# Kernel tuning notes

Hardware: AMD Instinct MI355X
Metric: run time of the kernel (lower is better)

## Reference

```python
import jax, jax.numpy as jnp
import numpy as np

B, LQ, LK, H = 4, 256, 512, 256

def setup_inputs() -> dict:
    key = jax.random.key(0)
    ks = jax.random.split(key, 9)
    return {
        "query": jax.random.normal(ks[0], (B, LQ, H), dtype=jnp.float32),
        "key": jax.random.normal(ks[1], (B, LK, H), dtype=jnp.float32),
        "value": jax.random.normal(ks[2], (B, LK, H), dtype=jnp.float32),
        "mask": jax.random.randint(ks[3], (B, LK), 0, 2, dtype=jnp.int32),
        "Wq": jax.random.normal(ks[4], (H, H), dtype=jnp.float32) / np.sqrt(H),
        "bq": jnp.zeros((H,), dtype=jnp.float32),
        "Wk": jax.random.normal(ks[5], (H, H), dtype=jnp.float32) / np.sqrt(H),
        "bk": jnp.zeros((H,), dtype=jnp.float32),
        "v": jax.random.normal(ks[6], (H,), dtype=jnp.float32) / np.sqrt(H),
        "bv": jnp.zeros((), dtype=jnp.float32),
    }

def reference(query, key, value, mask, Wq, bq, Wk, bk, v, bv):
    # Linear projections: y = x @ W^T + b (torch nn.Linear convention)
    q = query @ Wq.T + bq            # [B, Lq, H]
    k = key @ Wk.T + bk              # [B, Lk, H]
    # Broadcast add -> tanh -> project to scalar with v
    s = jnp.tanh(q[:, :, None, :] + k[:, None, :, :])   # [B, Lq, Lk, H]
    scores = jnp.einsum('bqkh,h->bqk', s, v) + bv        # [B, Lq, Lk]
    scores = jnp.where(mask[:, None, :] == 0, -jnp.inf, scores)
    attn_weights = jax.nn.softmax(scores, axis=-1)       # [B, Lq, Lk]
    attn_output = jnp.einsum('bqk,bkh->bqh', attn_weights, value)
    return (attn_output, attn_weights)
```

## Files before the change

### kernel.cpp

```cpp
#include <hip/hip_runtime.h>
#include <math.h>

#define NB  4
#define NLQ 256
#define NLK 512
#define NH  256

#define SCALE_2LOG2E 2.885390081777927f
#define LOG2E        1.4426950408889634f

__global__ __launch_bounds__(256) void setup_kernel(
    const float* __restrict__ Wq, const float* __restrict__ Wk,
    const int* __restrict__ mask,
    float* __restrict__ Wtq, float* __restrict__ Wtk,
    int* __restrict__ act, int* __restrict__ nact)
{
    const int blk = blockIdx.x;
    const int t   = threadIdx.x;

    if (blk < 32) {
        __shared__ float ts[64][65];
        const int m    = blk >> 4;
        const int tile = blk & 15;
        const int h0 = (tile >> 2) * 64;
        const int c0 = (tile & 3) * 64;
        const float* W  = m ? Wk  : Wq;
        float*       Wt = m ? Wtk : Wtq;
        const int lr = t >> 4, lc = t & 15;
        #pragma unroll
        for (int i = 0; i < 4; ++i) {
            const int r = lr + 16 * i;
            const float4 d = *(const float4*)(W + (size_t)(h0 + r) * NH + c0 + lc * 4);
            ts[r][lc * 4 + 0] = d.x;
            ts[r][lc * 4 + 1] = d.y;
            ts[r][lc * 4 + 2] = d.z;
            ts[r][lc * 4 + 3] = d.w;
        }
        __syncthreads();
        #pragma unroll
        for (int i = 0; i < 4; ++i) {
            const int c = lr + 16 * i;
            float4 d;
            d.x = ts[lc * 4 + 0][c];
            d.y = ts[lc * 4 + 1][c];
            d.z = ts[lc * 4 + 2][c];
            d.w = ts[lc * 4 + 3][c];
            *(float4*)(Wt + (size_t)(c0 + c) * NH + h0 + lc * 4) = d;
        }
    } else if (blk < 32 + NB) {
        const int b = blk - 32;
        __shared__ int wcnt[8], wpre[9];
        const int lane = t & 63, wave = t >> 6;
        const int k1 = t, k2 = t + 256;
        const int m1 = mask[b * NLK + k1];
        const int m2 = mask[b * NLK + k2];
        const unsigned long long below = (1ULL << lane) - 1ULL;
        const unsigned long long bal1 = __ballot(m1 != 0);
        const unsigned long long bal2 = __ballot(m2 != 0);
        const int r1 = __popcll(bal1 & below);
        const int r2 = __popcll(bal2 & below);
        if (lane == 0) { wcnt[wave] = __popcll(bal1); wcnt[4 + wave] = __popcll(bal2); }
        __syncthreads();
        if (t == 0) {
            int s = 0;
            #pragma unroll
            for (int w = 0; w < 8; ++w) { wpre[w] = s; s += wcnt[w]; }
            wpre[8] = s;
        }
        __syncthreads();
        const int na = wpre[8];
        if (m1) act[b * NLK + wpre[wave]     + r1] = k1;
        if (m2) act[b * NLK + wpre[4 + wave] + r2] = k2;
        if (k1 >= na) act[b * NLK + k1] = 0;
        if (k2 >= na) act[b * NLK + k2] = 0;
        if (t == 0) nact[b] = na;
    }
}

__global__ __launch_bounds__(256) void prep_kernel(
    const float* __restrict__ query, const float* __restrict__ key,
    const float* __restrict__ Wtq, const float* __restrict__ bq,
    const float* __restrict__ Wtk, const float* __restrict__ bk,
    const int* __restrict__ act, const int* __restrict__ nact,
    float* __restrict__ qp, float* __restrict__ kp_ct)
{
    const int blk  = blockIdx.x;
    const int t    = threadIdx.x;
    const int wave = t >> 6;
    const int lane = t & 63;

    __shared__ float  xs[4][NH];
    __shared__ float4 ps[4][4][64];
    __shared__ int    ridx[4];

    const float *Wt, *bias;
    int b = 0, j0 = 0, r0 = 0, na = 0;
    const bool isq = (blk < NB * NLQ / 4);

    if (isq) {
        b  = blk & 3;
        r0 = b * NLQ + (blk >> 2) * 4;
        ((float4*)&xs[0][0])[t] = ((const float4*)(query + (size_t)r0 * NH))[t];
        Wt = Wtq; bias = bq;
    } else {
        const int idx = blk - 256;
        b  = idx & 3;
        j0 = (idx >> 2) * 4;
        na = nact[b];
        if (j0 >= na) return;
        if (t < 4) ridx[t] = act[b * NLK + ((j0 + t < na) ? (j0 + t) : j0)];
        __syncthreads();
        const int r = t >> 6, c4 = t & 63;
        ((float4*)xs[r])[c4] =
            ((const float4*)(key + ((size_t)b * NLK + ridx[r]) * NH))[c4];
        Wt = Wtk; bias = bk;
    }
    __syncthreads();

    float4 acc[4];
    #pragma unroll
    for (int r = 0; r < 4; ++r) acc[r] = (float4){0.f, 0.f, 0.f, 0.f};

    const int cbase = wave * 64;
    #pragma unroll 4
    for (int cc = 0; cc < 64; ++cc) {
        const int c = cbase + cc;
        const float4 w = *(const float4*)(Wt + (size_t)c * NH + lane * 4);
        #pragma unroll
        for (int r = 0; r < 4; ++r) {
            const float xv = xs[r][c];
            acc[r].x = fmaf(xv, w.x, acc[r].x);
            acc[r].y = fmaf(xv, w.y, acc[r].y);
            acc[r].z = fmaf(xv, w.z, acc[r].z);
            acc[r].w = fmaf(xv, w.w, acc[r].w);
        }
    }
    #pragma unroll
    for (int r = 0; r < 4; ++r) ps[wave][r][lane] = acc[r];
    __syncthreads();

    const int r = wave, l = lane;
    const float4 p0 = ps[0][r][l], p1 = ps[1][r][l];
    const float4 p2 = ps[2][r][l], p3 = ps[3][r][l];
    const float4 bb = *(const float4*)(bias + l * 4);
    float4 o;
    o.x = (p0.x + p1.x + p2.x + p3.x + bb.x) * SCALE_2LOG2E;
    o.y = (p0.y + p1.y + p2.y + p3.y + bb.y) * SCALE_2LOG2E;
    o.z = (p0.z + p1.z + p2.z + p3.z + bb.z) * SCALE_2LOG2E;
    o.w = (p0.w + p1.w + p2.w + p3.w + bb.w) * SCALE_2LOG2E;
    o.x = __builtin_amdgcn_exp2f(o.x);
    o.y = __builtin_amdgcn_exp2f(o.y);
    o.z = __builtin_amdgcn_exp2f(o.z);
    o.w = __builtin_amdgcn_exp2f(o.w);

    if (isq) {
        *(float4*)(qp + (size_t)(r0 + r) * NH + l * 4) = o;
    } else if (j0 + r < na) {
        const int j = j0 + r;
        kp_ct[((size_t)b * NH + l * 4 + 0) * NLK + j] = o.x;
        kp_ct[((size_t)b * NH + l * 4 + 1) * NLK + j] = o.y;
        kp_ct[((size_t)b * NH + l * 4 + 2) * NLK + j] = o.z;
        kp_ct[((size_t)b * NH + l * 4 + 3) * NLK + j] = o.w;
    }
}

__global__ __launch_bounds__(512) void attn_kernel(
    const float* __restrict__ qp, const float* __restrict__ kp_ct,
    const float* __restrict__ value, const int* __restrict__ mask,
    const int* __restrict__ act, const int* __restrict__ nact,
    const float* __restrict__ vvec,
    float* __restrict__ out_o, float* __restrict__ out_w)
{
    __shared__ float sc0[NLK], sc1[NLK];
    __shared__ int   actl[NLK];
    __shared__ float eqs[2][NH];
    __shared__ float vvs[NH];
    __shared__ float4 buf4[2048];

    const int blk  = blockIdx.x;
    const int b    = blk & 3;
    const int q0   = (blk >> 2) * 2;
    const int t    = threadIdx.x;
    const int lane = t & 63;
    const int wave = t >> 6;

    const int na = nact[b];
    actl[t] = (t < na) ? act[b * NLK + t] : 0;
    if (t < NH) {
        eqs[0][t] = qp[(size_t)(b * NLQ + q0) * NH + t];
        eqs[1][t] = qp[(size_t)(b * NLQ + q0 + 1) * NH + t];
        vvs[t]    = vvec[t];
    }

    float* w0row = out_w + (size_t)(b * NLQ + q0) * NLK;
    float* w1row = w0row + NLK;
    if (!mask[b * NLK + t]) { w0row[t] = 0.f; w1row[t] = 0.f; }
    __syncthreads();

    const int cb = wave * 32;
    const float* kb  = kp_ct + ((size_t)b * NH + cb) * NLK;
    const float* eq0 = &eqs[0][cb];
    const float* eq1 = &eqs[1][cb];
    const float* vv  = &vvs[cb];

    float4 a0 = {0.f, 0.f, 0.f, 0.f}, a1 = {0.f, 0.f, 0.f, 0.f};
    float4 a2 = {0.f, 0.f, 0.f, 0.f}, a3 = {0.f, 0.f, 0.f, 0.f};
    if (na > 256) {
        #pragma unroll 4
        for (int c = 0; c < 32; ++c) {
            const float4 k1 = *(const float4*)(kb + (size_t)c * NLK + 4 * lane);
            const float4 k2 = *(const float4*)(kb + (size_t)c * NLK + 256 + 4 * lane);
            const float eqa = eq0[c];
            const float eqb = eq1[c];
            const float vh  = vv[c];
            a0.x = fmaf(vh, __builtin_amdgcn_rcpf(fmaf(eqa, k1.x, 1.f)), a0.x);
            a0.y = fmaf(vh, __builtin_amdgcn_rcpf(fmaf(eqa, k1.y, 1.f)), a0.y);
            a0.z = fmaf(vh, __builtin_amdgcn_rcpf(fmaf(eqa, k1.z, 1.f)), a0.z);
            a0.w = fmaf(vh, __builtin_amdgcn_rcpf(fmaf(eqa, k1.w, 1.f)), a0.w);
            a1.x = fmaf(vh, __builtin_amdgcn_rcpf(fmaf(eqb, k1.x, 1.f)), a1.x);
            a1.y = fmaf(vh, __builtin_amdgcn_rcpf(fmaf(eqb, k1.y, 1.f)), a1.y);
            a1.z = fmaf(vh, __builtin_amdgcn_rcpf(fmaf(eqb, k1.z, 1.f)), a1.z);
            a1.w = fmaf(vh, __builtin_amdgcn_rcpf(fmaf(eqb, k1.w, 1.f)), a1.w);
            a2.x = fmaf(vh, __builtin_amdgcn_rcpf(fmaf(eqa, k2.x, 1.f)), a2.x);
            a2.y = fmaf(vh, __builtin_amdgcn_rcpf(fmaf(eqa, k2.y, 1.f)), a2.y);
            a2.z = fmaf(vh, __builtin_amdgcn_rcpf(fmaf(eqa, k2.z, 1.f)), a2.z);
            a2.w = fmaf(vh, __builtin_amdgcn_rcpf(fmaf(eqa, k2.w, 1.f)), a2.w);
            a3.x = fmaf(vh, __builtin_amdgcn_rcpf(fmaf(eqb, k2.x, 1.f)), a3.x);
            a3.y = fmaf(vh, __builtin_amdgcn_rcpf(fmaf(eqb, k2.y, 1.f)), a3.y);
            a3.z = fmaf(vh, __builtin_amdgcn_rcpf(fmaf(eqb, k2.z, 1.f)), a3.z);
            a3.w = fmaf(vh, __builtin_amdgcn_rcpf(fmaf(eqb, k2.w, 1.f)), a3.w);
        }
    } else {
        #pragma unroll 4
        for (int c = 0; c < 32; ++c) {
            const float4 k1 = *(const float4*)(kb + (size_t)c * NLK + 4 * lane);
            const float eqa = eq0[c];
            const float eqb = eq1[c];
            const float vh  = vv[c];
            a0.x = fmaf(vh, __builtin_amdgcn_rcpf(fmaf(eqa, k1.x, 1.f)), a0.x);
            a0.y = fmaf(vh, __builtin_amdgcn_rcpf(fmaf(eqa, k1.y, 1.f)), a0.y);
            a0.z = fmaf(vh, __builtin_amdgcn_rcpf(fmaf(eqa, k1.z, 1.f)), a0.z);
            a0.w = fmaf(vh, __builtin_amdgcn_rcpf(fmaf(eqa, k1.w, 1.f)), a0.w);
            a1.x = fmaf(vh, __builtin_amdgcn_rcpf(fmaf(eqb, k1.x, 1.f)), a1.x);
            a1.y = fmaf(vh, __builtin_amdgcn_rcpf(fmaf(eqb, k1.y, 1.f)), a1.y);
            a1.z = fmaf(vh, __builtin_amdgcn_rcpf(fmaf(eqb, k1.z, 1.f)), a1.z);
            a1.w = fmaf(vh, __builtin_amdgcn_rcpf(fmaf(eqb, k1.w, 1.f)), a1.w);
        }
    }
    buf4[(0 * 8 + wave) * 128 + lane]      = a0;
    buf4[(0 * 8 + wave) * 128 + 64 + lane] = a2;
    buf4[(1 * 8 + wave) * 128 + lane]      = a1;
    buf4[(1 * 8 + wave) * 128 + 64 + lane] = a3;
    __syncthreads();
    {
        const float* pf = (const float*)buf4;
        float sA = 0.f, sB = 0.f;
        #pragma unroll
        for (int o = 0; o < 8; ++o) {
            sA += pf[o * 512 + t];
            sB += pf[(8 + o) * 512 + t];
        }
        sc0[t] = (t < na) ? -2.f * sA : -INFINITY;
        sc1[t] = (t < na) ? -2.f * sB : -INFINITY;
    }
    __syncthreads();

    if (wave < 2) {
        float* row = wave ? sc1 : sc0;
        float vals[8];
        float m = -INFINITY;
        #pragma unroll
        for (int j8 = 0; j8 < 8; ++j8) {
            vals[j8] = row[lane + j8 * 64];
            m = fmaxf(m, vals[j8]);
        }
        #pragma unroll
        for (int s = 32; s >= 1; s >>= 1)
            m = fmaxf(m, __shfl_xor(m, s, 64));
        float sum = 0.0f;
        #pragma unroll
        for (int j8 = 0; j8 < 8; ++j8) {
            vals[j8] = __builtin_amdgcn_exp2f((vals[j8] - m) * LOG2E);
            sum += vals[j8];
        }
        #pragma unroll
        for (int s = 32; s >= 1; s >>= 1)
            sum += __shfl_xor(sum, s, 64);
        const float inv = __builtin_amdgcn_rcpf(sum);
        float* wout = out_w + (size_t)(b * NLQ + q0 + wave) * NLK;
        #pragma unroll
        for (int j8 = 0; j8 < 8; ++j8) {
            const int jj = lane + j8 * 64;
            const float w = vals[j8] * inv;
            row[jj] = w;
            if (jj < na) wout[actl[jj]] = w;
        }
    }
    __syncthreads();

    {
        const int c4 = lane * 4;
        const float* vb = value + (size_t)b * NLK * NH + c4;
        float4 o0 = {0.f, 0.f, 0.f, 0.f}, o1 = {0.f, 0.f, 0.f, 0.f};
        #pragma unroll 4
        for (int j = wave; j < na; j += 8) {
            const float w0 = sc0[j];
            const float w1 = sc1[j];
            const int   rj = actl[j];
            const float4 v4 = *(const float4*)(vb + (size_t)rj * NH);
            o0.x = fmaf(w0, v4.x, o0.x); o0.y = fmaf(w0, v4.y, o0.y);
            o0.z = fmaf(w0, v4.z, o0.z); o0.w = fmaf(w0, v4.w, o0.w);
            o1.x = fmaf(w1, v4.x, o1.x); o1.y = fmaf(w1, v4.y, o1.y);
            o1.z = fmaf(w1, v4.z, o1.z); o1.w = fmaf(w1, v4.w, o1.w);
        }
        buf4[t]       = o0;
        buf4[512 + t] = o1;
        __syncthreads();
        if (t < 128) {
            const int row = t >> 6;
            const int l   = t & 63;
            float4 o = buf4[row * 512 + l];
            #pragma unroll
            for (int w = 1; w < 8; ++w) {
                const float4 s = buf4[row * 512 + l + 64 * w];
                o.x += s.x; o.y += s.y; o.z += s.z; o.w += s.w;
            }
            *(float4*)(out_o + (size_t)(b * NLQ + q0 + row) * NH + l * 4) = o;
        }
    }
}

extern "C" void kernel_launch(void* const* d_in, const int* in_sizes, int n_in,
                              void* d_out, int out_size, void* d_ws, size_t ws_size,
                              hipStream_t stream) {
    const float* query = (const float*)d_in[0];
    const float* key   = (const float*)d_in[1];
    const float* value = (const float*)d_in[2];
    const int*   mask  = (const int*)  d_in[3];
    const float* Wq    = (const float*)d_in[4];
    const float* bq    = (const float*)d_in[5];
    const float* Wk    = (const float*)d_in[6];
    const float* bk    = (const float*)d_in[7];
    const float* v     = (const float*)d_in[8];

    float* out_o = (float*)d_out;
    float* out_w = out_o + NB * NLQ * NH;

    float* qp    = (float*)d_ws;
    float* kp_ct = qp + NB * NLQ * NH;
    int*   act   = (int*)(kp_ct + NB * NH * NLK);
    int*   nact  = act + NB * NLK;

    const size_t base = (size_t)(NB * NLQ * NH) + (size_t)(NB * NH * NLK)
                      + NB * NLK + NB;
    float* wtq;
    if (ws_size >= (base + 2 * NH * NH) * sizeof(float)) {
        wtq = (float*)d_ws + base;
    } else {
        wtq = out_w + (size_t)NB * NLQ * NLK - 2 * NH * NH;
    }
    float* wtk = wtq + NH * NH;

    setup_kernel<<<36, 256, 0, stream>>>(Wq, Wk, mask, wtq, wtk, act, nact);
    prep_kernel<<<NB * NLQ / 4 + NB * NLK / 4, 256, 0, stream>>>(
        query, key, wtq, bq, wtk, bk, act, nact, qp, kp_ct);
    attn_kernel<<<NB * NLQ / 2, 512, 0, stream>>>(
        qp, kp_ct, value, mask, act, nact, v, out_o, out_w);
}
```

Before: 106.8 us.

## Process one query row per attention block instead of two

The attention kernel now handles a single query row per block and launches twice as many blocks. Each block does half the tanh/score work and uses half the shared memory and accumulator registers, which should raise occupancy and spread work across more CUs. In exchange, each block still reloads the full projected-key tile and the value rows, so global/L2 traffic for keys and values doubles. An extra barrier is also added before the output reduction buffer is reused.

```diff
diff --git a/kernel.cpp b/kernel.cpp
--- a/kernel.cpp
+++ b/kernel.cpp
@@ -171,15 +171,15 @@
     const float* __restrict__ vvec,
     float* __restrict__ out_o, float* __restrict__ out_w)
 {
-    __shared__ float sc0[NLK], sc1[NLK];
+    __shared__ float sc[NLK];
     __shared__ int   actl[NLK];
-    __shared__ float eqs[2][NH];
+    __shared__ float eqs[NH];
     __shared__ float vvs[NH];
-    __shared__ float4 buf4[2048];
+    __shared__ float4 buf4[1024];
 
     const int blk  = blockIdx.x;
     const int b    = blk & 3;
-    const int q0   = (blk >> 2) * 2;
+    const int q    = blk >> 2;
     const int t    = threadIdx.x;
     const int lane = t & 63;
     const int wave = t >> 6;
@@ -187,91 +187,68 @@
     const int na = nact[b];
     actl[t] = (t < na) ? act[b * NLK + t] : 0;
     if (t < NH) {
-        eqs[0][t] = qp[(size_t)(b * NLQ + q0) * NH + t];
-        eqs[1][t] = qp[(size_t)(b * NLQ + q0 + 1) * NH + t];
-        vvs[t]    = vvec[t];
-    }
-
-    float* w0row = out_w + (size_t)(b * NLQ + q0) * NLK;
-    float* w1row = w0row + NLK;
-    if (!mask[b * NLK + t]) { w0row[t] = 0.f; w1row[t] = 0.f; }
+        eqs[t] = qp[(size_t)(b * NLQ + q) * NH + t];
+        vvs[t] = vvec[t];
+    }
+
+    float* wrow = out_w + (size_t)(b * NLQ + q) * NLK;
+    if (!mask[b * NLK + t]) wrow[t] = 0.f;
     __syncthreads();
 
     const int cb = wave * 32;
-    const float* kb  = kp_ct + ((size_t)b * NH + cb) * NLK;
-    const float* eq0 = &eqs[0][cb];
-    const float* eq1 = &eqs[1][cb];
-    const float* vv  = &vvs[cb];
-
-    float4 a0 = {0.f, 0.f, 0.f, 0.f}, a1 = {0.f, 0.f, 0.f, 0.f};
-    float4 a2 = {0.f, 0.f, 0.f, 0.f}, a3 = {0.f, 0.f, 0.f, 0.f};
+    const float* kb = kp_ct + ((size_t)b * NH + cb) * NLK;
+    const float* eq = &eqs[cb];
+    const float* vv = &vvs[cb];
+
+    float4 a0 = {0.f, 0.f, 0.f, 0.f};
+    float4 a1 = {0.f, 0.f, 0.f, 0.f};
     if (na > 256) {
         #pragma unroll 4
         for (int c = 0; c < 32; ++c) {
             const float4 k1 = *(const float4*)(kb + (size_t)c * NLK + 4 * lane);
             const float4 k2 = *(const float4*)(kb + (size_t)c * NLK + 256 + 4 * lane);
-            const float eqa = eq0[c];
-            const float eqb = eq1[c];
-            const float vh  = vv[c];
-            a0.x = fmaf(vh, __builtin_amdgcn_rcpf(fmaf(eqa, k1.x, 1.f)), a0.x);
-            a0.y = fmaf(vh, __builtin_amdgcn_rcpf(fmaf(eqa, k1.y, 1.f)), a0.y);
-            a0.z = fmaf(vh, __builtin_amdgcn_rcpf(fmaf(eqa, k1.z, 1.f)), a0.z);
-            a0.w = fmaf(vh, __builtin_amdgcn_rcpf(fmaf(eqa, k1.w, 1.f)), a0.w);
-            a1.x = fmaf(vh, __builtin_amdgcn_rcpf(fmaf(eqb, k1.x, 1.f)), a1.x);
-            a1.y = fmaf(vh, __builtin_amdgcn_rcpf(fmaf(eqb, k1.y, 1.f)), a1.y);
-            a1.z = fmaf(vh, __builtin_amdgcn_rcpf(fmaf(eqb, k1.z, 1.f)), a1.z);
-            a1.w = fmaf(vh, __builtin_amdgcn_rcpf(fmaf(eqb, k1.w, 1.f)), a1.w);
-            a2.x = fmaf(vh, __builtin_amdgcn_rcpf(fmaf(eqa, k2.x, 1.f)), a2.x);
-            a2.y = fmaf(vh, __builtin_amdgcn_rcpf(fmaf(eqa, k2.y, 1.f)), a2.y);
-            a2.z = fmaf(vh, __builtin_amdgcn_rcpf(fmaf(eqa, k2.z, 1.f)), a2.z);
-            a2.w = fmaf(vh, __builtin_amdgcn_rcpf(fmaf(eqa, k2.w, 1.f)), a2.w);
-            a3.x = fmaf(vh, __builtin_amdgcn_rcpf(fmaf(eqb, k2.x, 1.f)), a3.x);
-            a3.y = fmaf(vh, __builtin_amdgcn_rcpf(fmaf(eqb, k2.y, 1.f)), a3.y);
-            a3.z = fmaf(vh, __builtin_amdgcn_rcpf(fmaf(eqb, k2.z, 1.f)), a3.z);
-            a3.w = fmaf(vh, __builtin_amdgcn_rcpf(fmaf(eqb, k2.w, 1.f)), a3.w);
+            const float e  = eq[c];
+            const float vh = vv[c];
+            a0.x = fmaf(vh, __builtin_amdgcn_rcpf(fmaf(e, k1.x, 1.f)), a0.x);
+            a0.y = fmaf(vh, __builtin_amdgcn_rcpf(fmaf(e, k1.y, 1.f)), a0.y);
+            a0.z = fmaf(vh, __builtin_amdgcn_rcpf(fmaf(e, k1.z, 1.f)), a0.z);
+            a0.w = fmaf(vh, __builtin_amdgcn_rcpf(fmaf(e, k1.w, 1.f)), a0.w);
+            a1.x = fmaf(vh, __builtin_amdgcn_rcpf(fmaf(e, k2.x, 1.f)), a1.x);
+            a1.y = fmaf(vh, __builtin_amdgcn_rcpf(fmaf(e, k2.y, 1.f)), a1.y);
+            a1.z = fmaf(vh, __builtin_amdgcn_rcpf(fmaf(e, k2.z, 1.f)), a1.z);
+            a1.w = fmaf(vh, __builtin_amdgcn_rcpf(fmaf(e, k2.w, 1.f)), a1.w);
         }
     } else {
         #pragma unroll 4
         for (int c = 0; c < 32; ++c) {
             const float4 k1 = *(const float4*)(kb + (size_t)c * NLK + 4 * lane);
-            const float eqa = eq0[c];
-            const float eqb = eq1[c];
-            const float vh  = vv[c];
-            a0.x = fmaf(vh, __builtin_amdgcn_rcpf(fmaf(eqa, k1.x, 1.f)), a0.x);
-            a0.y = fmaf(vh, __builtin_amdgcn_rcpf(fmaf(eqa, k1.y, 1.f)), a0.y);
-            a0.z = fmaf(vh, __builtin_amdgcn_rcpf(fmaf(eqa, k1.z, 1.f)), a0.z);
-            a0.w = fmaf(vh, __builtin_amdgcn_rcpf(fmaf(eqa, k1.w, 1.f)), a0.w);
-            a1.x = fmaf(vh, __builtin_amdgcn_rcpf(fmaf(eqb, k1.x, 1.f)), a1.x);
-            a1.y = fmaf(vh, __builtin_amdgcn_rcpf(fmaf(eqb, k1.y, 1.f)), a1.y);
-            a1.z = fmaf(vh, __builtin_amdgcn_rcpf(fmaf(eqb, k1.z, 1.f)), a1.z);
-            a1.w = fmaf(vh, __builtin_amdgcn_rcpf(fmaf(eqb, k1.w, 1.f)), a1.w);
-        }
-    }
-    buf4[(0 * 8 + wave) * 128 + lane]      = a0;
-    buf4[(0 * 8 + wave) * 128 + 64 + lane] = a2;
-    buf4[(1 * 8 + wave) * 128 + lane]      = a1;
-    buf4[(1 * 8 + wave) * 128 + 64 + lane] = a3;
-    __syncthreads();
+            const float e  = eq[c];
+            const float vh = vv[c];
+            a0.x = fmaf(vh, __builtin_amdgcn_rcpf(fmaf(e, k1.x, 1.f)), a0.x);
+            a0.y = fmaf(vh, __builtin_amdgcn_rcpf(fmaf(e, k1.y, 1.f)), a0.y);
+            a0.z = fmaf(vh, __builtin_amdgcn_rcpf(fmaf(e, k1.z, 1.f)), a0.z);
+            a0.w = fmaf(vh, __builtin_amdgcn_rcpf(fmaf(e, k1.w, 1.f)), a0.w);
+        }
+    }
+    buf4[wave * 128 + lane]      = a0;
+    buf4[wave * 128 + 64 + lane] = a1;
+    __syncthreads();
+
     {
         const float* pf = (const float*)buf4;
-        float sA = 0.f, sB = 0.f;
-        #pragma unroll
-        for (int o = 0; o < 8; ++o) {
-            sA += pf[o * 512 + t];
-            sB += pf[(8 + o) * 512 + t];
-        }
-        sc0[t] = (t < na) ? -2.f * sA : -INFINITY;
-        sc1[t] = (t < na) ? -2.f * sB : -INFINITY;
-    }
-    __syncthreads();
-
-    if (wave < 2) {
-        float* row = wave ? sc1 : sc0;
+        float s = 0.f;
+        #pragma unroll
+        for (int o = 0; o < 8; ++o) s += pf[o * 512 + t];
+        sc[t] = (t < na) ? -2.f * s : -INFINITY;
+    }
+    __syncthreads();
+
+    if (wave == 0) {
         float vals[8];
         float m = -INFINITY;
         #pragma unroll
         for (int j8 = 0; j8 < 8; ++j8) {
-            vals[j8] = row[lane + j8 * 64];
+            vals[j8] = sc[lane + j8 * 64];
             m = fmaxf(m, vals[j8]);
         }
         #pragma unroll
@@ -287,45 +264,38 @@
         for (int s = 32; s >= 1; s >>= 1)
             sum += __shfl_xor(sum, s, 64);
         const float inv = __builtin_amdgcn_rcpf(sum);
-        float* wout = out_w + (size_t)(b * NLQ + q0 + wave) * NLK;
         #pragma unroll
         for (int j8 = 0; j8 < 8; ++j8) {
             const int jj = lane + j8 * 64;
             const float w = vals[j8] * inv;
-            row[jj] = w;
-            if (jj < na) wout[actl[jj]] = w;
+            sc[jj] = w;
+            if (jj < na) wrow[actl[jj]] = w;
         }
     }
     __syncthreads();
 
     {
-        const int c4 = lane * 4;
-        const float* vb = value + (size_t)b * NLK * NH + c4;
-        float4 o0 = {0.f, 0.f, 0.f, 0.f}, o1 = {0.f, 0.f, 0.f, 0.f};
+        const float* vb = value + (size_t)b * NLK * NH + lane * 4;
+        float4 o0 = {0.f, 0.f, 0.f, 0.f};
         #pragma unroll 4
         for (int j = wave; j < na; j += 8) {
-            const float w0 = sc0[j];
-            const float w1 = sc1[j];
+            const float w0 = sc[j];
             const int   rj = actl[j];
             const float4 v4 = *(const float4*)(vb + (size_t)rj * NH);
             o0.x = fmaf(w0, v4.x, o0.x); o0.y = fmaf(w0, v4.y, o0.y);
             o0.z = fmaf(w0, v4.z, o0.z); o0.w = fmaf(w0, v4.w, o0.w);
-            o1.x = fmaf(w1, v4.x, o1.x); o1.y = fmaf(w1, v4.y, o1.y);
-            o1.z = fmaf(w1, v4.z, o1.z); o1.w = fmaf(w1, v4.w, o1.w);
-        }
-        buf4[t]       = o0;
-        buf4[512 + t] = o1;
-        __syncthreads();
-        if (t < 128) {
-            const int row = t >> 6;
-            const int l   = t & 63;
-            float4 o = buf4[row * 512 + l];
+        }
+        __syncthreads();
+        buf4[t] = o0;
+        __syncthreads();
+        if (t < 64) {
+            float4 o = buf4[t];
             #pragma unroll
             for (int w = 1; w < 8; ++w) {
-                const float4 s = buf4[row * 512 + l + 64 * w];
+                const float4 s = buf4[w * 64 + t];
                 o.x += s.x; o.y += s.y; o.z += s.z; o.w += s.w;
             }
-            *(float4*)(out_o + (size_t)(b * NLQ + q0 + row) * NH + l * 4) = o;
+            *(float4*)(out_o + (size_t)(b * NLQ + q) * NH + t * 4) = o;
         }
     }
 }
@@ -364,6 +334,6 @@
     setup_kernel<<<36, 256, 0, stream>>>(Wq, Wk, mask, wtq, wtk, act, nact);
     prep_kernel<<<NB * NLQ / 4 + NB * NLK / 4, 256, 0, stream>>>(
         query, key, wtq, bq, wtk, bk, act, nact, qp, kp_ct);
-    attn_kernel<<<NB * NLQ / 2, 512, 0, stream>>>(
+    attn_kernel<<<NB * NLQ, 512, 0, stream>>>(
         qp, kp_ct, value, mask, act, nact, v, out_o, out_w);
 }
```

After: 113.9 us. 1.07x slower.

## Pair hidden channels to share one reciprocal and add mid-size active-key path

Applied to the files above, without the earlier changes.

Combines two terms v_a/d_a + v_b/d_b into (v_b*d_a + v_a*d_b)/(d_a*d_b), so each pair of hidden channels needs one transcendental reciprocal instead of two. This trades the rcp cost for extra multiplies and FMAs. It also adds a path for 257–320 active keys that loads only one scalar for the overflow columns instead of a full second float4 block. A barrier is inserted before the shared buffer is reused, and the pairwise product may change rounding or overflow behaviour.

```diff
diff --git a/kernel.cpp b/kernel.cpp
--- a/kernel.cpp
+++ b/kernel.cpp
@@ -164,6 +164,12 @@
     }
 }
 
+#define PR(acc_, eA_, kA_, eB_, kB_, vA_, vB_) {                               \
+    const float da_ = fmaf(eA_, kA_, 1.f);                                     \
+    const float db_ = fmaf(eB_, kB_, 1.f);                                     \
+    const float nm_ = fmaf(vB_, da_, vA_ * db_);                               \
+    acc_ = fmaf(nm_, __builtin_amdgcn_rcpf(da_ * db_), acc_); }
+
 __global__ __launch_bounds__(512) void attn_kernel(
     const float* __restrict__ qp, const float* __restrict__ kp_ct,
     const float* __restrict__ value, const int* __restrict__ mask,
@@ -204,53 +210,84 @@
     const float* vv  = &vvs[cb];
 
     float4 a0 = {0.f, 0.f, 0.f, 0.f}, a1 = {0.f, 0.f, 0.f, 0.f};
-    float4 a2 = {0.f, 0.f, 0.f, 0.f}, a3 = {0.f, 0.f, 0.f, 0.f};
-    if (na > 256) {
+    if (na > 256 && na <= 320) {
+        float ov0 = 0.f, ov1 = 0.f;
         #pragma unroll 4
-        for (int c = 0; c < 32; ++c) {
-            const float4 k1 = *(const float4*)(kb + (size_t)c * NLK + 4 * lane);
-            const float4 k2 = *(const float4*)(kb + (size_t)c * NLK + 256 + 4 * lane);
-            const float eqa = eq0[c];
-            const float eqb = eq1[c];
-            const float vh  = vv[c];
-            a0.x = fmaf(vh, __builtin_amdgcn_rcpf(fmaf(eqa, k1.x, 1.f)), a0.x);
-            a0.y = fmaf(vh, __builtin_amdgcn_rcpf(fmaf(eqa, k1.y, 1.f)), a0.y);
-            a0.z = fmaf(vh, __builtin_amdgcn_rcpf(fmaf(eqa, k1.z, 1.f)), a0.z);
-            a0.w = fmaf(vh, __builtin_amdgcn_rcpf(fmaf(eqa, k1.w, 1.f)), a0.w);
-            a1.x = fmaf(vh, __builtin_amdgcn_rcpf(fmaf(eqb, k1.x, 1.f)), a1.x);
-            a1.y = fmaf(vh, __builtin_amdgcn_rcpf(fmaf(eqb, k1.y, 1.f)), a1.y);
-            a1.z = fmaf(vh, __builtin_amdgcn_rcpf(fmaf(eqb, k1.z, 1.f)), a1.z);
-            a1.w = fmaf(vh, __builtin_amdgcn_rcpf(fmaf(eqb, k1.w, 1.f)), a1.w);
-            a2.x = fmaf(vh, __builtin_amdgcn_rcpf(fmaf(eqa, k2.x, 1.f)), a2.x);
-            a2.y = fmaf(vh, __builtin_amdgcn_rcpf(fmaf(eqa, k2.y, 1.f)), a2.y);
-            a2.z = fmaf(vh, __builtin_amdgcn_rcpf(fmaf(eqa, k2.z, 1.f)), a2.z);
-            a2.w = fmaf(vh, __builtin_amdgcn_rcpf(fmaf(eqa, k2.w, 1.f)), a2.w);
-            a3.x = fmaf(vh, __builtin_amdgcn_rcpf(fmaf(eqb, k2.x, 1.f)), a3.x);
-            a3.y = fmaf(vh, __builtin_amdgcn_rcpf(fmaf(eqb, k2.y, 1.f)), a3.y);
-            a3.z = fmaf(vh, __builtin_amdgcn_rcpf(fmaf(eqb, k2.z, 1.f)), a3.z);
-            a3.w = fmaf(vh, __builtin_amdgcn_rcpf(fmaf(eqb, k2.w, 1.f)), a3.w);
-        }
+        for (int c = 0; c < 32; c += 2) {
+            const float4 kA = *(const float4*)(kb + (size_t)c * NLK + 4 * lane);
+            const float4 kB = *(const float4*)(kb + (size_t)(c + 1) * NLK + 4 * lane);
+            const float koA = kb[(size_t)c * NLK + 256 + lane];
+            const float koB = kb[(size_t)(c + 1) * NLK + 256 + lane];
+            const float e0A = eq0[c], e0B = eq0[c + 1];
+            const float e1A = eq1[c], e1B = eq1[c + 1];
+            const float vA  = vv[c],  vB  = vv[c + 1];
+            PR(a0.x, e0A, kA.x, e0B, kB.x, vA, vB)
+            PR(a0.y, e0A, kA.y, e0B, kB.y, vA, vB)
+            PR(a0.z, e0A, kA.z, e0B, kB.z, vA, vB)
+            PR(a0.w, e0A, kA.w, e0B, kB.w, vA, vB)
+            PR(a1.x, e1A, kA.x, e1B, kB.x, vA, vB)
+            PR(a1.y, e1A, kA.y, e1B, kB.y, vA, vB)
+            PR(a1.z, e1A, kA.z, e1B, kB.z, vA, vB)
+            PR(a1.w, e1A, kA.w, e1B, kB.w, vA, vB)
+            PR(ov0,  e0A, koA,  e0B, koB,  vA, vB)
+            PR(ov1,  e1A, koA,  e1B, koB,  vA, vB)
+        }
+        buf4[(0 * 8 + wave) * 128 + lane] = a0;
+        buf4[(1 * 8 + wave) * 128 + lane] = a1;
+        ((float*)buf4)[(0 * 8 + wave) * 512 + 256 + lane] = ov0;
+        ((float*)buf4)[(1 * 8 + wave) * 512 + 256 + lane] = ov1;
+    } else if (na > 320) {
+        float4 a2 = {0.f, 0.f, 0.f, 0.f}, a3 = {0.f, 0.f, 0.f, 0.f};
+        #pragma unroll 2
+        for (int c = 0; c < 32; c += 2) {
+            const float4 kA  = *(const float4*)(kb + (size_t)c * NLK + 4 * lane);
+            const float4 kB  = *(const float4*)(kb + (size_t)(c + 1) * NLK + 4 * lane);
+            const float4 k2A = *(const float4*)(kb + (size_t)c * NLK + 256 + 4 * lane);
+            const float4 k2B = *(const float4*)(kb + (size_t)(c + 1) * NLK + 256 + 4 * lane);
+            const float e0A = eq0[c], e0B = eq0[c + 1];
+            const float e1A = eq1[c], e1B = eq1[c + 1];
+            const float vA  = vv[c],  vB  = vv[c + 1];
+            PR(a0.x, e0A, kA.x,  e0B, kB.x,  vA, vB)
+            PR(a0.y, e0A, kA.y,  e0B, kB.y,  vA, vB)
+            PR(a0.z, e0A, kA.z,  e0B, kB.z,  vA, vB)
+            PR(a0.w, e0A, kA.w,  e0B, kB.w,  vA, vB)
+            PR(a1.x, e1A, kA.x,  e1B, kB.x,  vA, vB)
+            PR(a1.y, e1A, kA.y,  e1B, kB.y,  vA, vB)
+            PR(a1.z, e1A, kA.z,  e1B, kB.z,  vA, vB)
+            PR(a1.w, e1A, kA.w,  e1B, kB.w,  vA, vB)
+            PR(a2.x, e0A, k2A.x, e0B, k2B.x, vA, vB)
+            PR(a2.y, e0A, k2A.y, e0B, k2B.y, vA, vB)
+            PR(a2.z, e0A, k2A.z, e0B, k2B.z, vA, vB)
+            PR(a2.w, e0A, k2A.w, e0B, k2B.w, vA, vB)
+            PR(a3.x, e1A, k2A.x, e1B, k2B.x, vA, vB)
+            PR(a3.y, e1A, k2A.y, e1B, k2B.y, vA, vB)
+            PR(a3.z, e1A, k2A.z, e1B, k2B.z, vA, vB)
+            PR(a3.w, e1A, k2A.w, e1B, k2B.w, vA, vB)
+        }
+        buf4[(0 * 8 + wave) * 128 + lane]      = a0;
+        buf4[(0 * 8 + wave) * 128 + 64 + lane] = a2;
+        buf4[(1 * 8 + wave) * 128 + lane]      = a1;
+        buf4[(1 * 8 + wave) * 128 + 64 + lane] = a3;
     } else {
         #pragma unroll 4
-        for (int c = 0; c < 32; ++c) {
-            const float4 k1 = *(const float4*)(kb + (size_t)c * NLK + 4 * lane);
-            const float eqa = eq0[c];
-            const float eqb = eq1[c];
-            const float vh  = vv[c];
-            a0.x = fmaf(vh, __builtin_amdgcn_rcpf(fmaf(eqa, k1.x, 1.f)), a0.x);
-            a0.y = fmaf(vh, __builtin_amdgcn_rcpf(fmaf(eqa, k1.y, 1.f)), a0.y);
-            a0.z = fmaf(vh, __builtin_amdgcn_rcpf(fmaf(eqa, k1.z, 1.f)), a0.z);
-            a0.w = fmaf(vh, __builtin_amdgcn_rcpf(fmaf(eqa, k1.w, 1.f)), a0.w);
-            a1.x = fmaf(vh, __builtin_amdgcn_rcpf(fmaf(eqb, k1.x, 1.f)), a1.x);
-            a1.y = fmaf(vh, __builtin_amdgcn_rcpf(fmaf(eqb, k1.y, 1.f)), a1.y);
-            a1.z = fmaf(vh, __builtin_amdgcn_rcpf(fmaf(eqb, k1.z, 1.f)), a1.z);
-            a1.w = fmaf(vh, __builtin_amdgcn_rcpf(fmaf(eqb, k1.w, 1.f)), a1.w);
-        }
-    }
-    buf4[(0 * 8 + wave) * 128 + lane]      = a0;
-    buf4[(0 * 8 + wave) * 128 + 64 + lane] = a2;
-    buf4[(1 * 8 + wave) * 128 + lane]      = a1;
-    buf4[(1 * 8 + wave) * 128 + 64 + lane] = a3;
+        for (int c = 0; c < 32; c += 2) {
+            const float4 kA = *(const float4*)(kb + (size_t)c * NLK + 4 * lane);
+            const float4 kB = *(const float4*)(kb + (size_t)(c + 1) * NLK + 4 * lane);
+            const float e0A = eq0[c], e0B = eq0[c + 1];
+            const float e1A = eq1[c], e1B = eq1[c + 1];
+            const float vA  = vv[c],  vB  = vv[c + 1];
+            PR(a0.x, e0A, kA.x, e0B, kB.x, vA, vB)
+            PR(a0.y, e0A, kA.y, e0B, kB.y, vA, vB)
+            PR(a0.z, e0A, kA.z, e0B, kB.z, vA, vB)
+            PR(a0.w, e0A, kA.w, e0B, kB.w, vA, vB)
+            PR(a1.x, e1A, kA.x, e1B, kB.x, vA, vB)
+            PR(a1.y, e1A, kA.y, e1B, kB.y, vA, vB)
+            PR(a1.z, e1A, kA.z, e1B, kB.z, vA, vB)
+            PR(a1.w, e1A, kA.w, e1B, kB.w, vA, vB)
+        }
+        buf4[(0 * 8 + wave) * 128 + lane] = a0;
+        buf4[(1 * 8 + wave) * 128 + lane] = a1;
+    }
     __syncthreads();
     {
         const float* pf = (const float*)buf4;
@@ -313,6 +350,7 @@
             o1.x = fmaf(w1, v4.x, o1.x); o1.y = fmaf(w1, v4.y, o1.y);
             o1.z = fmaf(w1, v4.z, o1.z); o1.w = fmaf(w1, v4.w, o1.w);
         }
+        __syncthreads();
         buf4[t]       = o0;
         buf4[512 + t] = o1;
         __syncthreads();
```

Result: no change. 107.5 us (+0.7%).
